# Optimization experiments

Measured on AMD Instinct MI355X. Metric: run time of the kernel, lower is better.

Reference implementation:

```python
import jax, jax.numpy as jnp
import numpy as np

TAU = 2.0  # aggregator_temp


def setup_inputs() -> dict:
    key = jax.random.key(0)
    k1, k2 = jax.random.split(key)
    B, Na, Nv, D = 32, 512, 256, 384
    audio_feats = jax.random.normal(k1, (B, Na, D), dtype=jnp.float32)
    visual_feats = jax.random.normal(k2, (B, Nv, D), dtype=jnp.float32)
    return {"audio_feats": audio_feats, "visual_feats": visual_feats}


def reference(audio_feats, visual_feats):
    # Cross-batch token similarities: (B, B, Na, Nv)
    # token_sims[i, j, n, m] = <audio_feats[i, n], visual_feats[j, m]>
    token_sims = jnp.einsum('ind,jmd->ijnm', audio_feats, visual_feats)
    # logsumexp_pool: tau * logsumexp(sims / tau) over key-token dim (Nv),
    # then mean over query-token dim (Na) -> clip_sims (B, B)
    aggregator = TAU * jax.nn.logsumexp(token_sims / TAU, axis=-1)
    clip_sims = aggregator.mean(axis=-1)
    return clip_sims
```

## Files before the change

### kernel.cpp

```cpp
#include <hip/hip_runtime.h>

constexpr int B_  = 32;
constexpr int Na  = 512;
constexpr int Nv  = 256;
constexpr int D   = 384;

constexpr int NK2 = D / 64;

constexpr int AGROUPS = B_ * 16;
constexpr int BGROUPS = B_ * 8;
constexpr size_t GROUP_BYTES = 12 * 1024;
constexpr int SCALE_ONE = 0x7F7F7F7F;

typedef int   int4v    __attribute__((ext_vector_type(4)));
typedef int   int8v    __attribute__((ext_vector_type(8)));
typedef float floatx16 __attribute__((ext_vector_type(16)));

__device__ __forceinline__ void async_load16(const void* g, void* l) {
    __builtin_amdgcn_global_load_lds(
        (const __attribute__((address_space(1))) unsigned int*)g,
        (__attribute__((address_space(3))) unsigned int*)l,
        16, 0, 0);
}

__global__ void convert_fp8_kernel(const float* __restrict__ a, const float* __restrict__ v,
                                   unsigned char* __restrict__ a8,
                                   unsigned char* __restrict__ b8,
                                   float* __restrict__ out) {
    int gid = blockIdx.x * blockDim.x + threadIdx.x;
    if (gid < B_ * B_) out[gid] = 0.0f;

    const float* src;
    unsigned char* dst;
    int blk = blockIdx.x;
    const bool isA = blk < AGROUPS;
    if (isA) {
        src = a + (size_t)blk * 32 * D;
        dst = a8 + (size_t)blk * GROUP_BYTES;
    } else {
        int b2 = blk - AGROUPS;
        src = v + (size_t)b2 * 32 * D;
        dst = b8 + (size_t)b2 * GROUP_BYTES;
    }
    const int t = threadIdx.x;
    const int r = t >> 3, q = t & 7;

    #pragma unroll
    for (int p = 0; p < 3; ++p) {
        int k0 = p * 128 + q * 16;
        const float4* s4 = (const float4*)(src + (size_t)r * D + k0);
        float4 f0 = s4[0], f1 = s4[1], f2 = s4[2], f3 = s4[3];
        int w0 = 0, w1 = 0, w2 = 0, w3 = 0;
        w0 = __builtin_amdgcn_cvt_pk_fp8_f32(f0.x, f0.y, w0, false);
        w0 = __builtin_amdgcn_cvt_pk_fp8_f32(f0.z, f0.w, w0, true);
        w1 = __builtin_amdgcn_cvt_pk_fp8_f32(f1.x, f1.y, w1, false);
        w1 = __builtin_amdgcn_cvt_pk_fp8_f32(f1.z, f1.w, w1, true);
        w2 = __builtin_amdgcn_cvt_pk_fp8_f32(f2.x, f2.y, w2, false);
        w2 = __builtin_amdgcn_cvt_pk_fp8_f32(f2.z, f2.w, w2, true);
        w3 = __builtin_amdgcn_cvt_pk_fp8_f32(f3.x, f3.y, w3, false);
        w3 = __builtin_amdgcn_cvt_pk_fp8_f32(f3.z, f3.w, w3, true);
        int kc = k0 >> 5;
        int h2 = (k0 >> 4) & 1;
        size_t off;
        if (isA) {
            off = (size_t)kc * 1024 + h2 * 512 + r * 16;
        } else {
            int q2 = kc >> 1, u = kc & 1, l = r + 32 * h2;
            off = (size_t)q2 * 2048 + l * 32 + u * 16;
        }
        int4v o = { w0, w1, w2, w3 };
        *(int4v*)(dst + off) = o;
    }
}

__device__ __forceinline__ float expsum16(floatx16 a) {
    constexpr float INV_TAU_LN2 = 0.7213475204444817f;
    float e[16];
    #pragma unroll
    for (int i = 0; i < 16; ++i)
        e[i] = __builtin_amdgcn_exp2f(a[i] * INV_TAU_LN2);
    float t0 = (e[0] + e[1])  + (e[2] + e[3]);
    float t1 = (e[4] + e[5])  + (e[6] + e[7]);
    float t2 = (e[8] + e[9])  + (e[10] + e[11]);
    float t3 = (e[12] + e[13]) + (e[14] + e[15]);
    return (t0 + t1) + (t2 + t3);
}

__global__ __launch_bounds__(512, 4) void gemm_lse_kernel(
        const unsigned char* __restrict__ a8,
        const unsigned char* __restrict__ b8,
        float* __restrict__ out)
{
    __shared__ unsigned char ldsA[48 * 1024];
    __shared__ float ms[4][4][32];

    const int tid  = threadIdx.x;
    const int lane = tid & 63;
    const int wv   = tid >> 6;
    const int wm   = wv >> 2;
    const int wn   = wv & 3;

    int b = blockIdx.x;
    const int xcd   = b & 7;      b >>= 3;
    const int bi_lo = b & 3;      b >>= 2;
    const int rb    = b & 3;      b >>= 2;
    const int bj    = b;
    const int bi    = xcd * 4 + bi_lo;

    const unsigned char* asrc = a8 + (size_t)(bi * 16 + rb * 4) * GROUP_BYTES
                                   + (size_t)lane * 16;
    #pragma unroll
    for (int i = 0; i < 6; ++i) {
        const int u = wv * 6 + i;
        async_load16(asrc + (size_t)u * 1024, ldsA + u * 1024);
    }
    __syncthreads();

    const unsigned char* pv0 = b8 + (size_t)(bj * 8 + wn * 2) * GROUP_BYTES
                                  + (size_t)lane * 32;
    const unsigned char* pv1 = pv0 + GROUP_BYTES;
    const unsigned char* la  = ldsA + (size_t)(2 * wm) * GROUP_BYTES
                                    + (size_t)lane * 16;

    floatx16 acc[2][2];
    #pragma unroll
    for (int ag = 0; ag < 2; ++ag)
        #pragma unroll
        for (int vg = 0; vg < 2; ++vg)
            acc[ag][vg] = (floatx16)(0.0f);

    #pragma unroll
    for (int q2 = 0; q2 < NK2; ++q2) {
        int8v V0 = *(const int8v*)(pv0 + (size_t)q2 * 2048);
        int8v V1 = *(const int8v*)(pv1 + (size_t)q2 * 2048);
        int4v a0lo = *(const int4v*)(la + (size_t)q2 * 2048);
        int4v a0hi = *(const int4v*)(la + (size_t)q2 * 2048 + 1024);
        int4v a1lo = *(const int4v*)(la + GROUP_BYTES + (size_t)q2 * 2048);
        int4v a1hi = *(const int4v*)(la + GROUP_BYTES + (size_t)q2 * 2048 + 1024);
        int8v A0 = __builtin_shufflevector(a0lo, a0hi, 0, 1, 2, 3, 4, 5, 6, 7);
        int8v A1 = __builtin_shufflevector(a1lo, a1hi, 0, 1, 2, 3, 4, 5, 6, 7);
        __builtin_amdgcn_s_setprio(1);
        acc[0][0] = __builtin_amdgcn_mfma_scale_f32_32x32x64_f8f6f4(
            V0, A0, acc[0][0], 0, 0, 0, SCALE_ONE, 0, SCALE_ONE);
        acc[0][1] = __builtin_amdgcn_mfma_scale_f32_32x32x64_f8f6f4(
            V1, A0, acc[0][1], 0, 0, 0, SCALE_ONE, 0, SCALE_ONE);
        acc[1][0] = __builtin_amdgcn_mfma_scale_f32_32x32x64_f8f6f4(
            V0, A1, acc[1][0], 0, 0, 0, SCALE_ONE, 0, SCALE_ONE);
        acc[1][1] = __builtin_amdgcn_mfma_scale_f32_32x32x64_f8f6f4(
            V1, A1, acc[1][1], 0, 0, 0, SCALE_ONE, 0, SCALE_ONE);
        __builtin_amdgcn_s_setprio(0);
    }

    float s0 = expsum16(acc[0][0]) + expsum16(acc[0][1]);
    float s1 = expsum16(acc[1][0]) + expsum16(acc[1][1]);
    s0 += __shfl_xor(s0, 32);
    s1 += __shfl_xor(s1, 32);
    if (lane < 32) {
        ms[wn][2 * wm + 0][lane] = s0;
        ms[wn][2 * wm + 1][lane] = s1;
    }
    __syncthreads();

    if (tid < 128) {
        const int g = tid >> 5, r = tid & 31;
        float e = (ms[0][g][r] + ms[1][g][r]) + (ms[2][g][r] + ms[3][g][r]);
        constexpr float TAU_LN2 = 1.3862943611198906f;
        float lse = TAU_LN2 * __builtin_amdgcn_logf(e);
        #pragma unroll
        for (int m = 1; m < 64; m <<= 1) lse += __shfl_xor(lse, m);
        if ((tid & 63) == 0)
            atomicAdd(&out[bi * 32 + bj], lse * (1.0f / Na));
    }
}

extern "C" void kernel_launch(void* const* d_in, const int* in_sizes, int n_in,
                              void* d_out, int out_size, void* d_ws, size_t ws_size,
                              hipStream_t stream) {
    const float* audio  = (const float*)d_in[0];
    const float* visual = (const float*)d_in[1];
    float* out = (float*)d_out;

    unsigned char* a8 = (unsigned char*)d_ws;
    unsigned char* b8 = a8 + (size_t)AGROUPS * GROUP_BYTES;

    convert_fp8_kernel<<<dim3(AGROUPS + BGROUPS), dim3(256), 0, stream>>>(
        audio, visual, a8, b8, out);
    gemm_lse_kernel<<<dim3(4096), dim3(512), 0, stream>>>(a8, b8, out);
}
```

Measured before the change: 128.6 us.

## Double A-rows per block and prefetch visual fragments across K steps

Each block now covers 256 audio rows instead of 128, so every wave computes four A groups against the same two visual fragments, which halves the grid and the number of visual-operand global loads. The visual fragments for the next K step are loaded from global memory before the current MFMAs run, which is meant to hide load latency. This costs double the LDS (96KB) and more accumulator registers, and lowers the occupancy hint from 4 to 2 blocks per CU.

```diff
diff --git a/kernel.cpp b/kernel.cpp
--- a/kernel.cpp
+++ b/kernel.cpp
@@ -86,13 +86,13 @@
     return (t0 + t1) + (t2 + t3);
 }
 
-__global__ __launch_bounds__(512, 4) void gemm_lse_kernel(
+__global__ __launch_bounds__(512, 2) void gemm_lse_kernel(
         const unsigned char* __restrict__ a8,
         const unsigned char* __restrict__ b8,
         float* __restrict__ out)
 {
-    __shared__ unsigned char ldsA[48 * 1024];
-    __shared__ float ms[4][4][32];
+    __shared__ unsigned char ldsA[96 * 1024];
+    __shared__ float ms[4][8][32];
 
     const int tid  = threadIdx.x;
     const int lane = tid & 63;
@@ -103,65 +103,77 @@
     int b = blockIdx.x;
     const int xcd   = b & 7;      b >>= 3;
     const int bi_lo = b & 3;      b >>= 2;
-    const int rb    = b & 3;      b >>= 2;
+    const int rb    = b & 1;      b >>= 1;
     const int bj    = b;
     const int bi    = xcd * 4 + bi_lo;
 
-    const unsigned char* asrc = a8 + (size_t)(bi * 16 + rb * 4) * GROUP_BYTES
-                                   + (size_t)lane * 16;
-    #pragma unroll
-    for (int i = 0; i < 6; ++i) {
-        const int u = wv * 6 + i;
-        async_load16(asrc + (size_t)u * 1024, ldsA + u * 1024);
+    {
+        const unsigned char* gsrc = a8 + (size_t)(bi * 16 + rb * 8 + wv) * GROUP_BYTES
+                                       + (size_t)lane * 16;
+        unsigned char* ldst = ldsA + (size_t)wv * GROUP_BYTES;
+        #pragma unroll
+        for (int kc = 0; kc < 12; ++kc)
+            async_load16(gsrc + (size_t)kc * 1024, ldst + kc * 1024);
     }
     __syncthreads();
 
     const unsigned char* pv0 = b8 + (size_t)(bj * 8 + wn * 2) * GROUP_BYTES
                                   + (size_t)lane * 32;
     const unsigned char* pv1 = pv0 + GROUP_BYTES;
-    const unsigned char* la  = ldsA + (size_t)(2 * wm) * GROUP_BYTES
+    const unsigned char* la  = ldsA + (size_t)(wm * 4) * GROUP_BYTES
                                     + (size_t)lane * 16;
 
-    floatx16 acc[2][2];
-    #pragma unroll
-    for (int ag = 0; ag < 2; ++ag)
+    floatx16 acc[4][2];
+    #pragma unroll
+    for (int g = 0; g < 4; ++g)
         #pragma unroll
         for (int vg = 0; vg < 2; ++vg)
-            acc[ag][vg] = (floatx16)(0.0f);
+            acc[g][vg] = (floatx16)(0.0f);
+
+    int8v Vc0 = *(const int8v*)pv0;
+    int8v Vc1 = *(const int8v*)pv1;
 
     #pragma unroll
     for (int q2 = 0; q2 < NK2; ++q2) {
-        int8v V0 = *(const int8v*)(pv0 + (size_t)q2 * 2048);
-        int8v V1 = *(const int8v*)(pv1 + (size_t)q2 * 2048);
-        int4v a0lo = *(const int4v*)(la + (size_t)q2 * 2048);
-        int4v a0hi = *(const int4v*)(la + (size_t)q2 * 2048 + 1024);
-        int4v a1lo = *(const int4v*)(la + GROUP_BYTES + (size_t)q2 * 2048);
-        int4v a1hi = *(const int4v*)(la + GROUP_BYTES + (size_t)q2 * 2048 + 1024);
-        int8v A0 = __builtin_shufflevector(a0lo, a0hi, 0, 1, 2, 3, 4, 5, 6, 7);
-        int8v A1 = __builtin_shufflevector(a1lo, a1hi, 0, 1, 2, 3, 4, 5, 6, 7);
+        int8v Vn0, Vn1;
+        if (q2 + 1 < NK2) {
+            Vn0 = *(const int8v*)(pv0 + (size_t)(q2 + 1) * 2048);
+            Vn1 = *(const int8v*)(pv1 + (size_t)(q2 + 1) * 2048);
+        }
+        int8v A[4];
+        #pragma unroll
+        for (int g = 0; g < 4; ++g) {
+            const unsigned char* p = la + (size_t)g * GROUP_BYTES + (size_t)q2 * 2048;
+            int4v lo = *(const int4v*)p;
+            int4v hi = *(const int4v*)(p + 1024);
+            A[g] = __builtin_shufflevector(lo, hi, 0, 1, 2, 3, 4, 5, 6, 7);
+        }
         __builtin_amdgcn_s_setprio(1);
-        acc[0][0] = __builtin_amdgcn_mfma_scale_f32_32x32x64_f8f6f4(
-            V0, A0, acc[0][0], 0, 0, 0, SCALE_ONE, 0, SCALE_ONE);
-        acc[0][1] = __builtin_amdgcn_mfma_scale_f32_32x32x64_f8f6f4(
-            V1, A0, acc[0][1], 0, 0, 0, SCALE_ONE, 0, SCALE_ONE);
-        acc[1][0] = __builtin_amdgcn_mfma_scale_f32_32x32x64_f8f6f4(
-            V0, A1, acc[1][0], 0, 0, 0, SCALE_ONE, 0, SCALE_ONE);
-        acc[1][1] = __builtin_amdgcn_mfma_scale_f32_32x32x64_f8f6f4(
-            V1, A1, acc[1][1], 0, 0, 0, SCALE_ONE, 0, SCALE_ONE);
+        #pragma unroll
+        for (int g = 0; g < 4; ++g) {
+            acc[g][0] = __builtin_amdgcn_mfma_scale_f32_32x32x64_f8f6f4(
+                Vc0, A[g], acc[g][0], 0, 0, 0, SCALE_ONE, 0, SCALE_ONE);
+            acc[g][1] = __builtin_amdgcn_mfma_scale_f32_32x32x64_f8f6f4(
+                Vc1, A[g], acc[g][1], 0, 0, 0, SCALE_ONE, 0, SCALE_ONE);
+        }
         __builtin_amdgcn_s_setprio(0);
-    }
-
-    float s0 = expsum16(acc[0][0]) + expsum16(acc[0][1]);
-    float s1 = expsum16(acc[1][0]) + expsum16(acc[1][1]);
-    s0 += __shfl_xor(s0, 32);
-    s1 += __shfl_xor(s1, 32);
+        if (q2 + 1 < NK2) { Vc0 = Vn0; Vc1 = Vn1; }
+    }
+
+    float s[4];
+    #pragma unroll
+    for (int g = 0; g < 4; ++g) {
+        s[g] = expsum16(acc[g][0]) + expsum16(acc[g][1]);
+        s[g] += __shfl_xor(s[g], 32);
+    }
     if (lane < 32) {
-        ms[wn][2 * wm + 0][lane] = s0;
-        ms[wn][2 * wm + 1][lane] = s1;
+        #pragma unroll
+        for (int g = 0; g < 4; ++g)
+            ms[wn][wm * 4 + g][lane] = s[g];
     }
     __syncthreads();
 
-    if (tid < 128) {
+    if (tid < 256) {
         const int g = tid >> 5, r = tid & 31;
         float e = (ms[0][g][r] + ms[1][g][r]) + (ms[2][g][r] + ms[3][g][r]);
         constexpr float TAU_LN2 = 1.3862943611198906f;
@@ -185,5 +197,5 @@
 
     convert_fp8_kernel<<<dim3(AGROUPS + BGROUPS), dim3(256), 0, stream>>>(
         audio, visual, a8, b8, out);
-    gemm_lse_kernel<<<dim3(4096), dim3(512), 0, stream>>>(a8, b8, out);
-}
+    gemm_lse_kernel<<<dim3(2048), dim3(512), 0, stream>>>(a8, b8, out);
+}
```

After: 129.9 us. Within noise of the previous version (+1.0%).
